# Performance work log

Hardware: AMD Instinct MI355X
Metric: run time of the kernel (lower is better)

## Reference

```python
import jax, jax.numpy as jnp
import numpy as np

N_HEAD = 16
NEG_INF = jnp.float32(-1e30)


def setup_inputs() -> dict:
    key = jax.random.key(0)
    k1, k2, k3 = jax.random.split(key, 3)
    B, T, C = 2, 2048, 1024
    x = jax.random.normal(k1, (B, T, C), dtype=jnp.float32)
    attn_mask = jnp.ones((B, T), dtype=jnp.int32)
    W_qkv = jax.random.normal(k2, (C, 3 * C), dtype=jnp.float32) * (1.0 / np.sqrt(C))
    b_qkv = jnp.zeros((3 * C,), dtype=jnp.float32)
    W_proj = jax.random.normal(k3, (C, C), dtype=jnp.float32) * (1.0 / np.sqrt(C))
    b_proj = jnp.zeros((C,), dtype=jnp.float32)
    return {"x": x, "attn_mask": attn_mask, "W_qkv": W_qkv, "b_qkv": b_qkv,
            "W_proj": W_proj, "b_proj": b_proj}


def reference(x, attn_mask, W_qkv, b_qkv, W_proj, b_proj):
    B, T, C = x.shape
    H = N_HEAD
    hd = C // H
    qkv = x @ W_qkv + b_qkv                       # [B,T,3C]
    q, k, v = jnp.split(qkv, 3, axis=-1)
    q = q.reshape(B, T, H, hd).transpose(0, 2, 1, 3)  # [B,H,T,hd]
    k = k.reshape(B, T, H, hd).transpose(0, 2, 1, 3)
    v = v.reshape(B, T, H, hd).transpose(0, 2, 1, 3)
    att = jnp.einsum('bhqd,bhkd->bhqk', q, k) / jnp.float32(np.sqrt(hd))  # [B,H,T,T]
    causal = jnp.tril(jnp.ones((T, T), dtype=bool))[None, None]           # [1,1,T,T]
    pad = (attn_mask != 0)[:, None, None, :]                              # [B,1,1,T]
    att = jnp.where(causal & pad, att, NEG_INF)
    att = jax.nn.softmax(att, axis=-1)
    y = jnp.einsum('bhqk,bhkd->bhqd', att, v)     # [B,H,T,hd]
    y = y.transpose(0, 2, 1, 3).reshape(B, T, C)
    return y @ W_proj + b_proj
```

## Files before the change

### kernel.cpp

```cpp
#include <hip/hip_runtime.h>

#define T_SEQ 2048
#define NHEAD 16
#define HD 64
#define CDIM 1024

typedef __bf16 bf16x8 __attribute__((ext_vector_type(8)));
typedef float f32x4 __attribute__((ext_vector_type(4)));

union U16x8 { uint4 u4; unsigned short s[8]; bf16x8 b; };

__device__ __forceinline__ float bf2f(unsigned short u) {
    return __uint_as_float(((unsigned int)u) << 16);
}
__device__ __forceinline__ unsigned short f2bf(float f) {
    unsigned int u = __float_as_uint(f);
    u += 0x7fffu + ((u >> 16) & 1u);
    return (unsigned short)(u >> 16);
}
__device__ __forceinline__ unsigned short f2bf_fast(float f) {
    return (unsigned short)((__float_as_uint(f) + 0x8000u) >> 16);
}
__device__ __forceinline__ U16x8 load8f(const float* __restrict__ p) {
    U16x8 r;
    float4 f0 = *(const float4*)p;
    float4 f1 = *(const float4*)(p + 4);
    r.s[0] = f2bf(f0.x); r.s[1] = f2bf(f0.y); r.s[2] = f2bf(f0.z); r.s[3] = f2bf(f0.w);
    r.s[4] = f2bf(f1.x); r.s[5] = f2bf(f1.y); r.s[6] = f2bf(f1.z); r.s[7] = f2bf(f1.w);
    return r;
}

__device__ __forceinline__ void async_copy16(const unsigned short* g, unsigned short* l) {
    __builtin_amdgcn_global_load_lds(
        (const __attribute__((address_space(1))) unsigned int*)g,
        (__attribute__((address_space(3))) unsigned int*)l, 16, 0, 0);
}

#define LOG2E 1.442695040f

#define BAR()    asm volatile("s_barrier" ::: "memory")
#define LGKM0()  asm volatile("s_waitcnt lgkmcnt(0)" ::: "memory")
#define VMC6()   asm volatile("s_waitcnt vmcnt(6)" ::: "memory")
#define VMC0()   asm volatile("s_waitcnt vmcnt(0)" ::: "memory")

__global__ __launch_bounds__(256) void conv_bf16(
    const float* __restrict__ in, unsigned short* __restrict__ out, int n)
{
    const int i = (blockIdx.x * 256 + threadIdx.x) * 8;
    if (i < n) {
        U16x8 o = load8f(&in[i]);
        *(uint4*)&out[i] = o.u4;
    }
}

__global__ __launch_bounds__(256) void transpose_conv(
    const float* __restrict__ in, unsigned short* __restrict__ out, int R, int C)
{
    __shared__ float tile[64][65];
    const int r0 = blockIdx.x * 64;
    const int c0 = blockIdx.y * 64;
    const int tid = threadIdx.x;
    const int rr = tid >> 4;
    const int cc = (tid & 15) * 4;
#pragma unroll
    for (int p = 0; p < 4; ++p) {
        float4 v = *(const float4*)&in[(size_t)(r0 + p * 16 + rr) * C + c0 + cc];
        tile[p * 16 + rr][cc] = v.x;
        tile[p * 16 + rr][cc + 1] = v.y;
        tile[p * 16 + rr][cc + 2] = v.z;
        tile[p * 16 + rr][cc + 3] = v.w;
    }
    __syncthreads();
    const int n = tid >> 2;
    const int s = (tid & 3) * 8;
#pragma unroll
    for (int p = 0; p < 2; ++p) {
        const int k = s + p * 32;
        U16x8 o;
#pragma unroll
        for (int j = 0; j < 8; ++j) o.s[j] = f2bf(tile[k + j][n]);
        *(uint4*)&out[(size_t)(c0 + n) * R + r0 + k] = o.u4;
    }
}

__device__ __forceinline__ void gemm128_core(
    const unsigned short* __restrict__ A,
    const unsigned short* __restrict__ Bt,
    int K, int m0, int n0,
    unsigned short* As, unsigned short* Bs, f32x4 acc[4][4])
{
    const int tid = threadIdx.x;
    const int w = tid >> 6, lane = tid & 63;
    const int ln = lane & 15, quad = lane >> 4;
    const int wm = w >> 1, wn = w & 1;
    const int lr = lane >> 3;
    const int lc = (lane & 7) * 8;

    for (int kb = 0; kb < K; kb += 64) {
        __syncthreads();
#pragma unroll
        for (int i = 0; i < 4; ++i) {
            async_copy16(&A[(size_t)(m0 + w * 32 + i * 8 + lr) * K + kb + lc],
                         &As[(w * 32 + i * 8) * 64]);
            async_copy16(&Bt[(size_t)(n0 + w * 32 + i * 8 + lr) * K + kb + lc],
                         &Bs[(w * 32 + i * 8) * 64]);
        }
        __syncthreads();
#pragma unroll
        for (int kk = 0; kk < 2; ++kk) {
            U16x8 af[4], bff[4];
#pragma unroll
            for (int i = 0; i < 4; ++i)
                af[i].u4 = *(const uint4*)&As[(wm * 64 + i * 16 + ln) * 64 + kk * 32 + quad * 8];
#pragma unroll
            for (int j = 0; j < 4; ++j)
                bff[j].u4 = *(const uint4*)&Bs[(wn * 64 + j * 16 + ln) * 64 + kk * 32 + quad * 8];
#pragma unroll
            for (int i = 0; i < 4; ++i)
#pragma unroll
                for (int j = 0; j < 4; ++j)
                    acc[i][j] = __builtin_amdgcn_mfma_f32_16x16x32_bf16(af[i].b, bff[j].b, acc[i][j], 0, 0, 0);
        }
    }
}


__device__ __forceinline__ void stageA(const unsigned short* __restrict__ A,
                                       unsigned short* buf,
                                       int m0, int t, int unit, int w, int lane)
{
#pragma unroll
    for (int s = 0; s < 2; ++s) {
        const int r0 = s * 128 + unit * 64 + w * 8;
        const int row = r0 + (lane >> 3);
        const int col = (16 * (lane & 7)) ^ ((row & 4) ? 32 : 0);
        const unsigned short* src = A + (size_t)(m0 + row) * CDIM + t * 64 + (col >> 1);
        async_copy16(src, buf + r0 * 64);
    }
}

__device__ __forceinline__ void stageB(const unsigned short* __restrict__ B,
                                       unsigned short* buf,
                                       int n0, int t, int unit, int w, int lane)
{
#pragma unroll
    for (int s = 0; s < 2; ++s) {
        const int slice = s * 8 + w;
        const int r0 = (slice >> 2) * 64 + unit * 32 + (slice & 3) * 8;
        const int row = r0 + (lane >> 3);
        const int col = (16 * (lane & 7)) ^ ((row & 4) ? 32 : 0);
        const unsigned short* src = B + (size_t)(n0 + row) * CDIM + t * 64 + (col >> 1);
        async_copy16(src, buf + r0 * 64);
    }
}

__device__ __forceinline__ void readA(U16x8 af[4][2], const unsigned short* buf,
                                      int wm, int qm, int ln, int quad)
{
#pragma unroll
    for (int i = 0; i < 4; ++i) {
        const int row = wm * 128 + qm * 64 + i * 16 + ln;
        const int sw = (row & 4) ? 32 : 0;
#pragma unroll
        for (int kk = 0; kk < 2; ++kk) {
            const int byt = row * 128 + ((kk * 64 + quad * 16) ^ sw);
            af[i][kk].u4 = *(const uint4*)((const char*)buf + byt);
        }
    }
}

__device__ __forceinline__ void readB(U16x8 bf[2][2], const unsigned short* buf,
                                      int wn, int qn, int ln, int quad)
{
#pragma unroll
    for (int jj = 0; jj < 2; ++jj) {
        const int row = wn * 64 + qn * 32 + jj * 16 + ln;
        const int sw = (row & 4) ? 32 : 0;
#pragma unroll
        for (int kk = 0; kk < 2; ++kk) {
            const int byt = row * 128 + ((kk * 64 + quad * 16) ^ sw);
            bf[jj][kk].u4 = *(const uint4*)((const char*)buf + byt);
        }
    }
}

template<int QM, int QN>
__device__ __forceinline__ void mfma16(f32x4 acc[8][4], const U16x8 af[4][2],
                                       const U16x8 bf[2][2])
{
    __builtin_amdgcn_s_setprio(1);
#pragma unroll
    for (int i = 0; i < 4; ++i)
#pragma unroll
        for (int jj = 0; jj < 2; ++jj)
#pragma unroll
            for (int kk = 0; kk < 2; ++kk)
                acc[QM * 4 + i][QN * 2 + jj] = __builtin_amdgcn_mfma_f32_16x16x32_bf16(
                    af[i][kk].b, bf[jj][kk].b, acc[QM * 4 + i][QN * 2 + jj], 0, 0, 0);
    __builtin_amdgcn_s_setprio(0);
}

__global__ __launch_bounds__(512) void qkv8(
    const unsigned short* __restrict__ Xb,
    const unsigned short* __restrict__ Wt,
    const float* __restrict__ bias,
    unsigned short* __restrict__ Qp,
    unsigned short* __restrict__ Kp,
    unsigned short* __restrict__ Vtp)
{
    __shared__ __align__(1024) unsigned short smem[4][16384];
    unsigned short* Ab0 = smem[0];
    unsigned short* Ab1 = smem[1];
    unsigned short* Bb0 = smem[2];
    unsigned short* Bb1 = smem[3];

    const int tid = threadIdx.x;
    const int w = tid >> 6, lane = tid & 63;
    const int ln = lane & 15, quad = lane >> 4;
    const int wm = w >> 2, wn = w & 3;

    const int bid = blockIdx.x;
    const int swz = (bid & 7) * 24 + (bid >> 3);
    const int nt = swz % 12, mt = swz / 12;
    const int m0 = mt * 256, n0 = nt * 256;

    f32x4 acc[8][4];
#pragma unroll
    for (int i = 0; i < 8; ++i)
#pragma unroll
        for (int j = 0; j < 4; ++j) acc[i][j] = (f32x4){0.f, 0.f, 0.f, 0.f};

    stageA(Xb, Ab0, m0, 0, 0, w, lane);
    stageB(Wt, Bb0, n0, 0, 0, w, lane);
    stageB(Wt, Bb0, n0, 0, 1, w, lane);
    stageA(Xb, Ab0, m0, 0, 1, w, lane);
    stageA(Xb, Ab1, m0, 1, 0, w, lane);
    stageB(Wt, Bb1, n0, 1, 0, w, lane);
    stageB(Wt, Bb1, n0, 1, 1, w, lane);
    VMC6();
    BAR();

    U16x8 af[4][2], bq0[2][2], bq1[2][2];

    for (int j = 0; j < 7; ++j) {
        const int e = 2 * j, o = 2 * j + 1;
        readA(af, Ab0, wm, 0, ln, quad);
        readB(bq0, Bb0, wn, 0, ln, quad);
        stageA(Xb, Ab1, m0, o, 1, w, lane);
        BAR(); LGKM0();
        mfma16<0, 0>(acc, af, bq0);
        LGKM0(); BAR();
        readB(bq1, Bb0, wn, 1, ln, quad);
        stageA(Xb, Ab0, m0, e + 2, 0, w, lane);
        BAR(); LGKM0();
        mfma16<0, 1>(acc, af, bq1);
        LGKM0(); BAR();
        readA(af, Ab0, wm, 1, ln, quad);
        stageB(Wt, Bb0, n0, e + 2, 0, w, lane);
        BAR(); LGKM0();
        mfma16<1, 0>(acc, af, bq0);
        LGKM0(); BAR();
        stageB(Wt, Bb0, n0, e + 2, 1, w, lane);
        BAR();
        mfma16<1, 1>(acc, af, bq1);
        VMC6(); BAR();
        readA(af, Ab1, wm, 0, ln, quad);
        readB(bq0, Bb1, wn, 0, ln, quad);
        stageA(Xb, Ab0, m0, e + 2, 1, w, lane);
        BAR(); LGKM0();
        mfma16<0, 0>(acc, af, bq0);
        LGKM0(); BAR();
        readB(bq1, Bb1, wn, 1, ln, quad);
        stageA(Xb, Ab1, m0, o + 2, 0, w, lane);
        BAR(); LGKM0();
        mfma16<0, 1>(acc, af, bq1);
        LGKM0(); BAR();
        readA(af, Ab1, wm, 1, ln, quad);
        stageB(Wt, Bb1, n0, o + 2, 0, w, lane);
        BAR(); LGKM0();
        mfma16<1, 0>(acc, af, bq0);
        LGKM0(); BAR();
        stageB(Wt, Bb1, n0, o + 2, 1, w, lane);
        BAR();
        mfma16<1, 1>(acc, af, bq1);
        VMC6(); BAR();
    }

    stageA(Xb, Ab1, m0, 15, 1, w, lane);
    VMC0(); BAR();

    readA(af, Ab0, wm, 0, ln, quad);
    readB(bq0, Bb0, wn, 0, ln, quad);
    readB(bq1, Bb0, wn, 1, ln, quad);
    mfma16<0, 0>(acc, af, bq0);
    mfma16<0, 1>(acc, af, bq1);
    readA(af, Ab0, wm, 1, ln, quad);
    mfma16<1, 0>(acc, af, bq0);
    mfma16<1, 1>(acc, af, bq1);

    readA(af, Ab1, wm, 0, ln, quad);
    readB(bq0, Bb1, wn, 0, ln, quad);
    readB(bq1, Bb1, wn, 1, ln, quad);
    mfma16<0, 0>(acc, af, bq0);
    mfma16<0, 1>(acc, af, bq1);
    readA(af, Ab1, wm, 1, ln, quad);
    mfma16<1, 0>(acc, af, bq0);
    mfma16<1, 1>(acc, af, bq1);

    const int which = n0 >> 10;
    float bv[4];
#pragma unroll
    for (int jj = 0; jj < 4; ++jj) bv[jj] = bias[n0 + wn * 64 + jj * 16 + ln];

    if (which < 2) {
        unsigned short* dst = (which == 0) ? Qp : Kp;
#pragma unroll
        for (int jj = 0; jj < 4; ++jj) {
            const int n = n0 + wn * 64 + jj * 16 + ln;
            const int h = (n >> 6) & 15, d = n & 63;
#pragma unroll
            for (int i = 0; i < 8; ++i)
#pragma unroll
                for (int r = 0; r < 4; ++r) {
                    const int m = m0 + wm * 128 + i * 16 + quad * 4 + r;
                    const int b = m >> 11, tt = m & 2047;
                    dst[(((size_t)(b * NHEAD + h) * T_SEQ) + tt) * HD + d] =
                        f2bf(acc[i][jj][r] + bv[jj]);
                }
        }
    } else {
#pragma unroll
        for (int jj = 0; jj < 4; ++jj) {
            const int n = n0 + wn * 64 + jj * 16 + ln;
            const int c = n - 2048;
#pragma unroll
            for (int i = 0; i < 8; ++i) {
                const int m00 = m0 + wm * 128 + i * 16 + quad * 4;
                const int b = m00 >> 11, tt = m00 & 2047;
                ushort4 pk;
                pk.x = f2bf(acc[i][jj][0] + bv[jj]);
                pk.y = f2bf(acc[i][jj][1] + bv[jj]);
                pk.z = f2bf(acc[i][jj][2] + bv[jj]);
                pk.w = f2bf(acc[i][jj][3] + bv[jj]);
                *(ushort4*)&Vtp[(size_t)(b * 1024 + c) * T_SEQ + tt] = pk;
            }
        }
    }
}

__global__ __launch_bounds__(256) void proj_gemm(
    const unsigned short* __restrict__ Yin,
    const unsigned short* __restrict__ Wt,
    const float* __restrict__ bias,
    float* __restrict__ out)
{
    __shared__ unsigned short As[128 * 64];
    __shared__ unsigned short Bs[128 * 64];
    const int m0 = blockIdx.y * 128;
    const int n0 = blockIdx.x * 128;

    f32x4 acc[4][4];
#pragma unroll
    for (int i = 0; i < 4; ++i)
#pragma unroll
        for (int j = 0; j < 4; ++j) acc[i][j] = (f32x4){0.f, 0.f, 0.f, 0.f};

    gemm128_core(Yin, Wt, CDIM, m0, n0, As, Bs, acc);

    const int tid = threadIdx.x;
    const int w = tid >> 6, lane = tid & 63;
    const int ln = lane & 15, quad = lane >> 4;
    const int wm = w >> 1, wn = w & 1;

#pragma unroll
    for (int j = 0; j < 4; ++j) {
        const int n = n0 + wn * 64 + j * 16 + ln;
        const float bv = bias[n];
#pragma unroll
        for (int i = 0; i < 4; ++i)
#pragma unroll
            for (int r = 0; r < 4; ++r) {
                const int m = m0 + wm * 64 + i * 16 + quad * 4 + r;
                out[(size_t)m * CDIM + n] = acc[i][j][r] + bv;
            }
    }
}

#define ATT_STRIDE 72

__global__ __launch_bounds__(256) void flash_attn(
    const unsigned short* __restrict__ Qp,
    const unsigned short* __restrict__ Kp,
    const unsigned short* __restrict__ Vtp,
    const int* __restrict__ mask,
    unsigned short* __restrict__ Y)
{
    __shared__ unsigned short Ks[64 * ATT_STRIDE];
    __shared__ unsigned short Vs[64 * ATT_STRIDE];
    __shared__ unsigned short Ps[64 * ATT_STRIDE];
    __shared__ float mask_f[64];

    const int bh = blockIdx.x;
    const int qt = (T_SEQ / 64 - 1) - blockIdx.y;
    const int b = bh >> 4, h = bh & 15;
    const int tid = threadIdx.x;
    const int w = tid >> 6, lane = tid & 63;
    const int ln = lane & 15, quad = lane >> 4;
    const int row8 = tid >> 3, seg = tid & 7;
    const size_t base = (size_t)bh * T_SEQ * HD;
    const int q0 = qt * 64;

    U16x8 qf[2];
    {
        const unsigned short* qrow = &Qp[base + (size_t)(q0 + w * 16 + ln) * HD];
        qf[0].u4 = *(const uint4*)&qrow[quad * 8];
        qf[1].u4 = *(const uint4*)&qrow[32 + quad * 8];
    }

    f32x4 o[4];
#pragma unroll
    for (int n = 0; n < 4; ++n) o[n] = (f32x4){0.f, 0.f, 0.f, 0.f};
    float m_i[4] = {-3.0e38f, -3.0e38f, -3.0e38f, -3.0e38f};
    float l_i[4] = {0.f, 0.f, 0.f, 0.f};

    uint4 kr0, kr1, vr0, vr1;
    float mf = 0.f;
    {
        const unsigned short* kp0 = &Kp[base + (size_t)row8 * HD + seg * 8];
        kr0 = *(const uint4*)kp0;
        kr1 = *(const uint4*)(kp0 + 32 * HD);
        const unsigned short* vp0 = &Vtp[base + (size_t)row8 * T_SEQ + seg * 8];
        vr0 = *(const uint4*)vp0;
        vr1 = *(const uint4*)(vp0 + 32 * T_SEQ);
        if (tid < 64) mf = mask[b * T_SEQ + tid] ? 0.f : -1.0e30f;
    }

    for (int j = 0; j <= qt; ++j) {
        __syncthreads();
        *(uint4*)&Ks[row8 * ATT_STRIDE + seg * 8] = kr0;
        *(uint4*)&Ks[(row8 + 32) * ATT_STRIDE + seg * 8] = kr1;
        *(uint4*)&Vs[row8 * ATT_STRIDE + seg * 8] = vr0;
        *(uint4*)&Vs[(row8 + 32) * ATT_STRIDE + seg * 8] = vr1;
        if (tid < 64) mask_f[tid] = mf;
        __syncthreads();

        if (j < qt) {
            const unsigned short* kp0 = &Kp[base + (size_t)((j + 1) * 64 + row8) * HD + seg * 8];
            kr0 = *(const uint4*)kp0;
            kr1 = *(const uint4*)(kp0 + 32 * HD);
            const unsigned short* vp0 = &Vtp[base + (size_t)row8 * T_SEQ + (j + 1) * 64 + seg * 8];
            vr0 = *(const uint4*)vp0;
            vr1 = *(const uint4*)(vp0 + 32 * T_SEQ);
            if (tid < 64) mf = mask[b * T_SEQ + (j + 1) * 64 + tid] ? 0.f : -1.0e30f;
        }

        const bool diag = (j == qt);

        f32x4 sc[4];
#pragma unroll
        for (int t = 0; t < 4; ++t) sc[t] = (f32x4){0.f, 0.f, 0.f, 0.f};
#pragma unroll
        for (int t = 0; t < 4; ++t) {
            if (diag && t > w) continue;
#pragma unroll
            for (int s = 0; s < 2; ++s) {
                U16x8 kb;
                kb.u4 = *(const uint4*)&Ks[(t * 16 + ln) * ATT_STRIDE + s * 32 + quad * 8];
                sc[t] = __builtin_amdgcn_mfma_f32_16x16x32_bf16(qf[s].b, kb.b, sc[t], 0, 0, 0);
            }
        }

        float rm[4] = {-3.0e38f, -3.0e38f, -3.0e38f, -3.0e38f};
#pragma unroll
        for (int t = 0; t < 4; ++t) {
            if (diag && t > w) {
#pragma unroll
                for (int i = 0; i < 4; ++i) sc[t][i] = -1.0e30f;
            } else {
                const float madd = mask_f[t * 16 + ln];
                const bool edge = diag && (t == w);
#pragma unroll
                for (int i = 0; i < 4; ++i) {
                    float v = fmaf(sc[t][i], 0.125f, madd);
                    if (edge && ln > quad * 4 + i) v = -1.0e30f;
                    sc[t][i] = v;
                    rm[i] = fmaxf(rm[i], v);
                }
            }
        }
#pragma unroll
        for (int i = 0; i < 4; ++i) {
            rm[i] = fmaxf(rm[i], __shfl_xor(rm[i], 1));
            rm[i] = fmaxf(rm[i], __shfl_xor(rm[i], 2));
            rm[i] = fmaxf(rm[i], __shfl_xor(rm[i], 4));
            rm[i] = fmaxf(rm[i], __shfl_xor(rm[i], 8));
        }

        float alpha[4], mlog[4];
#pragma unroll
        for (int i = 0; i < 4; ++i) {
            const float nm = fmaxf(m_i[i], rm[i]);
            alpha[i] = __builtin_amdgcn_exp2f((m_i[i] - nm) * LOG2E);
            m_i[i] = nm;
            mlog[i] = nm * LOG2E;
        }
        float rsp[4] = {0.f, 0.f, 0.f, 0.f};
#pragma unroll
        for (int t = 0; t < 4; ++t)
#pragma unroll
            for (int i = 0; i < 4; ++i) {
                const float p = __builtin_amdgcn_exp2f(fmaf(sc[t][i], LOG2E, -mlog[i]));
                sc[t][i] = p;
                rsp[i] += p;
            }
#pragma unroll
        for (int i = 0; i < 4; ++i) l_i[i] = l_i[i] * alpha[i] + rsp[i];
#pragma unroll
        for (int n = 0; n < 4; ++n)
#pragma unroll
            for (int i = 0; i < 4; ++i) o[n][i] *= alpha[i];

#pragma unroll
        for (int t = 0; t < 4; ++t)
#pragma unroll
            for (int i = 0; i < 4; ++i)
                Ps[(w * 16 + quad * 4 + i) * ATT_STRIDE + t * 16 + ln] = f2bf_fast(sc[t][i]);

        U16x8 pa[2];
        pa[0].u4 = *(const uint4*)&Ps[(w * 16 + ln) * ATT_STRIDE + quad * 8];
        pa[1].u4 = *(const uint4*)&Ps[(w * 16 + ln) * ATT_STRIDE + 32 + quad * 8];

#pragma unroll
        for (int n = 0; n < 4; ++n)
#pragma unroll
            for (int s = 0; s < 2; ++s) {
                U16x8 vb;
                vb.u4 = *(const uint4*)&Vs[(n * 16 + ln) * ATT_STRIDE + s * 32 + quad * 8];
                o[n] = __builtin_amdgcn_mfma_f32_16x16x32_bf16(pa[s].b, vb.b, o[n], 0, 0, 0);
            }
    }

#pragma unroll
    for (int i = 0; i < 4; ++i) {
        float l = l_i[i];
        l += __shfl_xor(l, 1);
        l += __shfl_xor(l, 2);
        l += __shfl_xor(l, 4);
        l += __shfl_xor(l, 8);
        const float inv = 1.0f / l;
        const size_t row = (size_t)(b * T_SEQ + q0 + w * 16 + quad * 4 + i);
#pragma unroll
        for (int n = 0; n < 4; ++n)
            Y[row * CDIM + h * HD + n * 16 + ln] = f2bf(o[n][i] * inv);
    }
}

extern "C" void kernel_launch(void* const* d_in, const int* in_sizes, int n_in,
                              void* d_out, int out_size, void* d_ws, size_t ws_size,
                              hipStream_t stream)
{
    const float* X     = (const float*)d_in[0];
    const int*   mask  = (const int*)d_in[1];
    const float* Wqkv  = (const float*)d_in[2];
    const float* bqkv  = (const float*)d_in[3];
    const float* Wproj = (const float*)d_in[4];
    const float* bproj = (const float*)d_in[5];
    float* out = (float*)d_out;

    const size_t per = (size_t)2 * NHEAD * T_SEQ * HD;
    unsigned short* Qp     = (unsigned short*)d_ws;
    unsigned short* Kp     = Qp + per;
    unsigned short* Vtp    = Kp + per;
    unsigned short* Xb     = Vtp + per;
    unsigned short* Yp     = Xb;
    unsigned short* Wqkvt  = Xb + per;
    unsigned short* Wprojt = Wqkvt + (size_t)3 * CDIM * CDIM;

    conv_bf16<<<2048, 256, 0, stream>>>(X, Xb, 4 * 1024 * 1024);
    transpose_conv<<<dim3(16, 48), 256, 0, stream>>>(Wqkv, Wqkvt, CDIM, 3 * CDIM);
    transpose_conv<<<dim3(16, 16), 256, 0, stream>>>(Wproj, Wprojt, CDIM, CDIM);

    qkv8<<<192, 512, 0, stream>>>(Xb, Wqkvt, bqkv, Qp, Kp, Vtp);
    flash_attn<<<dim3(2 * NHEAD, T_SEQ / 64), 256, 0, stream>>>(Qp, Kp, Vtp, mask, Yp);
    proj_gemm<<<dim3(8, 32), 256, 0, stream>>>(Yp, Wprojt, bproj, out);
}
```

Before: 216.9 us.

## Rewrite flash attention with 32x32 MFMA, 128-row query tiles and register P

Replaces the flash attention kernel with one that processes 128 query rows per block (32 per wave) using 32x32x16 bf16 MFMA. It computes S^T so the probabilities can be packed to bf16 and moved into the A-operand layout with v_permlane32_swap, removing the LDS round trip for P. It also adds XOR-swizzled LDS for K/V, skips mask arithmetic when a ballot shows the tile is unmasked, and uses a lazy rescale that only updates the running max when it grows by more than 8. The grid shrinks to 512 blocks with fewer but longer blocks, which risks load imbalance and higher register pressure.

```diff
diff --git a/kernel.cpp b/kernel.cpp
--- a/kernel.cpp
+++ b/kernel.cpp
@@ -7,6 +7,7 @@
 
 typedef __bf16 bf16x8 __attribute__((ext_vector_type(8)));
 typedef float f32x4 __attribute__((ext_vector_type(4)));
+typedef float f32x16 __attribute__((ext_vector_type(16)));
 
 union U16x8 { uint4 u4; unsigned short s[8]; bf16x8 b; };
 
@@ -17,9 +18,6 @@
     unsigned int u = __float_as_uint(f);
     u += 0x7fffu + ((u >> 16) & 1u);
     return (unsigned short)(u >> 16);
-}
-__device__ __forceinline__ unsigned short f2bf_fast(float f) {
-    return (unsigned short)((__float_as_uint(f) + 0x8000u) >> 16);
 }
 __device__ __forceinline__ U16x8 load8f(const float* __restrict__ p) {
     U16x8 r;
@@ -43,6 +41,15 @@
 #define VMC6()   asm volatile("s_waitcnt vmcnt(6)" ::: "memory")
 #define VMC0()   asm volatile("s_waitcnt vmcnt(0)" ::: "memory")
 
+__device__ __forceinline__ unsigned int cvtpk_bf16(float lo, float hi) {
+    unsigned int r;
+    asm("v_cvt_pk_bf16_f32 %0, %1, %2" : "=v"(r) : "v"(lo), "v"(hi));
+    return r;
+}
+__device__ __forceinline__ void plane32swap(unsigned int &x, unsigned int &y) {
+    asm("v_permlane32_swap_b32 %0, %1" : "+v"(x), "+v"(y));
+}
+
 __global__ __launch_bounds__(256) void conv_bf16(
     const float* __restrict__ in, unsigned short* __restrict__ out, int n)
 {
@@ -123,7 +130,6 @@
         }
     }
 }
-
 
 __device__ __forceinline__ void stageA(const unsigned short* __restrict__ A,
                                        unsigned short* buf,
@@ -386,42 +392,49 @@
     }
 }
 
-#define ATT_STRIDE 72
-
-__global__ __launch_bounds__(256) void flash_attn(
+
+__device__ __forceinline__ int swz(int row, int slot) {
+    return row * 64 + ((slot ^ (row & 7)) << 3);
+}
+
+__global__ __launch_bounds__(256) void flash_attn32(
     const unsigned short* __restrict__ Qp,
     const unsigned short* __restrict__ Kp,
     const unsigned short* __restrict__ Vtp,
     const int* __restrict__ mask,
     unsigned short* __restrict__ Y)
 {
-    __shared__ unsigned short Ks[64 * ATT_STRIDE];
-    __shared__ unsigned short Vs[64 * ATT_STRIDE];
-    __shared__ unsigned short Ps[64 * ATT_STRIDE];
-    __shared__ float mask_f[64];
+    __shared__ unsigned short Ks[64 * 64];
+    __shared__ unsigned short Vs[64 * 64];
+    __shared__ float mask_arr[64];
+    __shared__ float als[4][32];
+    __shared__ int flagu;
 
     const int bh = blockIdx.x;
-    const int qt = (T_SEQ / 64 - 1) - blockIdx.y;
+    const int qb = 15 - blockIdx.y;
     const int b = bh >> 4, h = bh & 15;
     const int tid = threadIdx.x;
     const int w = tid >> 6, lane = tid & 63;
-    const int ln = lane & 15, quad = lane >> 4;
+    const int l31 = lane & 31, hi = lane >> 5;
     const int row8 = tid >> 3, seg = tid & 7;
     const size_t base = (size_t)bh * T_SEQ * HD;
-    const int q0 = qt * 64;
-
-    U16x8 qf[2];
+    const int qB = qb * 128;
+    const int qw0 = qB + w * 32;
+    const int qv = qw0 + l31;
+    const int jlast = 2 * qb + 1;
+
+    U16x8 qf[4];
     {
-        const unsigned short* qrow = &Qp[base + (size_t)(q0 + w * 16 + ln) * HD];
-        qf[0].u4 = *(const uint4*)&qrow[quad * 8];
-        qf[1].u4 = *(const uint4*)&qrow[32 + quad * 8];
-    }
-
-    f32x4 o[4];
-#pragma unroll
-    for (int n = 0; n < 4; ++n) o[n] = (f32x4){0.f, 0.f, 0.f, 0.f};
-    float m_i[4] = {-3.0e38f, -3.0e38f, -3.0e38f, -3.0e38f};
-    float l_i[4] = {0.f, 0.f, 0.f, 0.f};
+        const unsigned short* qrow = &Qp[base + (size_t)qv * HD];
+#pragma unroll
+        for (int c = 0; c < 4; ++c)
+            qf[c].u4 = *(const uint4*)&qrow[c * 16 + hi * 8];
+    }
+
+    f32x16 oA0, oA1;
+#pragma unroll
+    for (int r = 0; r < 16; ++r) { oA0[r] = 0.f; oA1[r] = 0.f; }
+    float m_r = -3.0e38f, mL = 0.f, l_r = 0.f;
 
     uint4 kr0, kr1, vr0, vr1;
     float mf = 0.f;
@@ -435,16 +448,22 @@
         if (tid < 64) mf = mask[b * T_SEQ + tid] ? 0.f : -1.0e30f;
     }
 
-    for (int j = 0; j <= qt; ++j) {
+    for (int j = 0; j <= jlast; ++j) {
         __syncthreads();
-        *(uint4*)&Ks[row8 * ATT_STRIDE + seg * 8] = kr0;
-        *(uint4*)&Ks[(row8 + 32) * ATT_STRIDE + seg * 8] = kr1;
-        *(uint4*)&Vs[row8 * ATT_STRIDE + seg * 8] = vr0;
-        *(uint4*)&Vs[(row8 + 32) * ATT_STRIDE + seg * 8] = vr1;
-        if (tid < 64) mask_f[tid] = mf;
+        *(uint4*)&Ks[swz(row8, seg)]      = kr0;
+        *(uint4*)&Ks[swz(row8 + 32, seg)] = kr1;
+        *(uint4*)&Vs[swz(row8, seg)]      = vr0;
+        *(uint4*)&Vs[swz(row8 + 32, seg)] = vr1;
+        if (w == 0) {
+            const int k = lane;
+            const int idx = ((k >> 2) & 1) * 32 + (k >> 5) * 16 + ((k & 31) >> 3) * 4 + (k & 3);
+            mask_arr[idx] = mf;
+            const unsigned long long bb = __ballot(mf == 0.f);
+            if (lane == 0) flagu = (bb == 0xFFFFFFFFFFFFFFFFull) ? 0 : 1;
+        }
         __syncthreads();
 
-        if (j < qt) {
+        if (j < jlast) {
             const unsigned short* kp0 = &Kp[base + (size_t)((j + 1) * 64 + row8) * HD + seg * 8];
             kr0 = *(const uint4*)kp0;
             kr1 = *(const uint4*)(kp0 + 32 * HD);
@@ -454,104 +473,129 @@
             if (tid < 64) mf = mask[b * T_SEQ + (j + 1) * 64 + tid] ? 0.f : -1.0e30f;
         }
 
-        const bool diag = (j == qt);
-
-        f32x4 sc[4];
-#pragma unroll
-        for (int t = 0; t < 4; ++t) sc[t] = (f32x4){0.f, 0.f, 0.f, 0.f};
-#pragma unroll
-        for (int t = 0; t < 4; ++t) {
-            if (diag && t > w) continue;
-#pragma unroll
-            for (int s = 0; s < 2; ++s) {
-                U16x8 kb;
-                kb.u4 = *(const uint4*)&Ks[(t * 16 + ln) * ATT_STRIDE + s * 32 + quad * 8];
-                sc[t] = __builtin_amdgcn_mfma_f32_16x16x32_bf16(qf[s].b, kb.b, sc[t], 0, 0, 0);
-            }
-        }
-
-        float rm[4] = {-3.0e38f, -3.0e38f, -3.0e38f, -3.0e38f};
-#pragma unroll
-        for (int t = 0; t < 4; ++t) {
-            if (diag && t > w) {
-#pragma unroll
-                for (int i = 0; i < 4; ++i) sc[t][i] = -1.0e30f;
+        const bool skipw = (j * 64 > qw0 + 31);
+        if (!skipw) {
+            const bool edge = (j * 64 + 63 > qw0);
+            const int anymask = flagu;
+
+            f32x16 sc0, sc1;
+#pragma unroll
+            for (int r = 0; r < 16; ++r) { sc0[r] = 0.f; sc1[r] = 0.f; }
+#pragma unroll
+            for (int c = 0; c < 4; ++c) {
+                U16x8 ka0, ka1;
+                const int r0 = l31, r1 = 32 + l31;
+                ka0.u4 = *(const uint4*)&Ks[r0 * 64 + (((2 * c + hi) ^ (r0 & 7)) << 3)];
+                ka1.u4 = *(const uint4*)&Ks[r1 * 64 + (((2 * c + hi) ^ (r1 & 7)) << 3)];
+                sc0 = __builtin_amdgcn_mfma_f32_32x32x16_bf16(ka0.b, qf[c].b, sc0, 0, 0, 0);
+                sc1 = __builtin_amdgcn_mfma_f32_32x32x16_bf16(ka1.b, qf[c].b, sc1, 0, 0, 0);
+            }
+
+            if (anymask) {
+#pragma unroll
+                for (int g = 0; g < 4; ++g) {
+                    const f32x4 m0v = *(const f32x4*)&mask_arr[hi * 32 + g * 4];
+                    const f32x4 m1v = *(const f32x4*)&mask_arr[hi * 32 + 16 + g * 4];
+#pragma unroll
+                    for (int t = 0; t < 4; ++t) {
+                        sc0[g * 4 + t] = fmaf(sc0[g * 4 + t], 0.125f, m0v[t]);
+                        sc1[g * 4 + t] = fmaf(sc1[g * 4 + t], 0.125f, m1v[t]);
+                    }
+                }
             } else {
-                const float madd = mask_f[t * 16 + ln];
-                const bool edge = diag && (t == w);
-#pragma unroll
-                for (int i = 0; i < 4; ++i) {
-                    float v = fmaf(sc[t][i], 0.125f, madd);
-                    if (edge && ln > quad * 4 + i) v = -1.0e30f;
-                    sc[t][i] = v;
-                    rm[i] = fmaxf(rm[i], v);
+#pragma unroll
+                for (int r = 0; r < 16; ++r) {
+                    sc0[r] *= 0.125f;
+                    sc1[r] *= 0.125f;
                 }
             }
-        }
-#pragma unroll
-        for (int i = 0; i < 4; ++i) {
-            rm[i] = fmaxf(rm[i], __shfl_xor(rm[i], 1));
-            rm[i] = fmaxf(rm[i], __shfl_xor(rm[i], 2));
-            rm[i] = fmaxf(rm[i], __shfl_xor(rm[i], 4));
-            rm[i] = fmaxf(rm[i], __shfl_xor(rm[i], 8));
-        }
-
-        float alpha[4], mlog[4];
-#pragma unroll
-        for (int i = 0; i < 4; ++i) {
-            const float nm = fmaxf(m_i[i], rm[i]);
-            alpha[i] = __builtin_amdgcn_exp2f((m_i[i] - nm) * LOG2E);
-            m_i[i] = nm;
-            mlog[i] = nm * LOG2E;
-        }
-        float rsp[4] = {0.f, 0.f, 0.f, 0.f};
-#pragma unroll
-        for (int t = 0; t < 4; ++t)
-#pragma unroll
-            for (int i = 0; i < 4; ++i) {
-                const float p = __builtin_amdgcn_exp2f(fmaf(sc[t][i], LOG2E, -mlog[i]));
-                sc[t][i] = p;
-                rsp[i] += p;
-            }
-#pragma unroll
-        for (int i = 0; i < 4; ++i) l_i[i] = l_i[i] * alpha[i] + rsp[i];
-#pragma unroll
-        for (int n = 0; n < 4; ++n)
-#pragma unroll
-            for (int i = 0; i < 4; ++i) o[n][i] *= alpha[i];
-
-#pragma unroll
-        for (int t = 0; t < 4; ++t)
-#pragma unroll
-            for (int i = 0; i < 4; ++i)
-                Ps[(w * 16 + quad * 4 + i) * ATT_STRIDE + t * 16 + ln] = f2bf_fast(sc[t][i]);
-
-        U16x8 pa[2];
-        pa[0].u4 = *(const uint4*)&Ps[(w * 16 + ln) * ATT_STRIDE + quad * 8];
-        pa[1].u4 = *(const uint4*)&Ps[(w * 16 + ln) * ATT_STRIDE + 32 + quad * 8];
-
-#pragma unroll
-        for (int n = 0; n < 4; ++n)
-#pragma unroll
-            for (int s = 0; s < 2; ++s) {
-                U16x8 vb;
-                vb.u4 = *(const uint4*)&Vs[(n * 16 + ln) * ATT_STRIDE + s * 32 + quad * 8];
-                o[n] = __builtin_amdgcn_mfma_f32_16x16x32_bf16(pa[s].b, vb.b, o[n], 0, 0, 0);
-            }
-    }
-
-#pragma unroll
-    for (int i = 0; i < 4; ++i) {
-        float l = l_i[i];
-        l += __shfl_xor(l, 1);
-        l += __shfl_xor(l, 2);
-        l += __shfl_xor(l, 4);
-        l += __shfl_xor(l, 8);
-        const float inv = 1.0f / l;
-        const size_t row = (size_t)(b * T_SEQ + q0 + w * 16 + quad * 4 + i);
-#pragma unroll
-        for (int n = 0; n < 4; ++n)
-            Y[row * CDIM + h * HD + n * 16 + ln] = f2bf(o[n][i] * inv);
+            if (edge) {
+#pragma unroll
+                for (int r = 0; r < 16; ++r) {
+                    const int krow = (r & 3) + 8 * (r >> 2) + 4 * hi;
+                    if (j * 64 + krow > qv)      sc0[r] = -1.0e30f;
+                    if (j * 64 + 32 + krow > qv) sc1[r] = -1.0e30f;
+                }
+            }
+
+            float tm = -3.0e38f;
+#pragma unroll
+            for (int r = 0; r < 16; ++r)
+                tm = fmaxf(tm, fmaxf(sc0[r], sc1[r]));
+            tm = fmaxf(tm, __shfl_xor(tm, 32));
+
+            if (__any(tm > m_r + 8.f)) {
+                const float mn = fmaxf(m_r, tm);
+                const float a = __builtin_amdgcn_exp2f((m_r - mn) * LOG2E);
+                m_r = mn; mL = mn * LOG2E;
+                l_r *= a;
+                if (hi == 0) als[w][l31] = a;
+                f32x4 av[4];
+#pragma unroll
+                for (int g = 0; g < 4; ++g)
+                    av[g] = *(const f32x4*)&als[w][g * 8 + hi * 4];
+#pragma unroll
+                for (int r = 0; r < 16; ++r) {
+                    const float aa = av[r >> 2][r & 3];
+                    oA0[r] *= aa; oA1[r] *= aa;
+                }
+            }
+
+            float ps = 0.f;
+#pragma unroll
+            for (int r = 0; r < 16; ++r) {
+                const float p0 = __builtin_amdgcn_exp2f(fmaf(sc0[r], LOG2E, -mL));
+                const float p1 = __builtin_amdgcn_exp2f(fmaf(sc1[r], LOG2E, -mL));
+                sc0[r] = p0; sc1[r] = p1;
+                ps += p0 + p1;
+            }
+            l_r += ps;
+
+#pragma unroll
+            for (int c = 0; c < 4; ++c) {
+                const int rb = (c & 1) * 8;
+                unsigned int x0, y0, x1, y1;
+                if (c < 2) {
+                    x0 = cvtpk_bf16(sc0[rb + 0], sc0[rb + 1]);
+                    y0 = cvtpk_bf16(sc0[rb + 4], sc0[rb + 5]);
+                    x1 = cvtpk_bf16(sc0[rb + 2], sc0[rb + 3]);
+                    y1 = cvtpk_bf16(sc0[rb + 6], sc0[rb + 7]);
+                } else {
+                    x0 = cvtpk_bf16(sc1[rb + 0], sc1[rb + 1]);
+                    y0 = cvtpk_bf16(sc1[rb + 4], sc1[rb + 5]);
+                    x1 = cvtpk_bf16(sc1[rb + 2], sc1[rb + 3]);
+                    y1 = cvtpk_bf16(sc1[rb + 6], sc1[rb + 7]);
+                }
+                plane32swap(x0, y0);
+                plane32swap(x1, y1);
+                U16x8 pa;
+                pa.u4 = make_uint4(x0, x1, y0, y1);
+                {
+                    const int vr_0 = l31, vr_1 = 32 + l31;
+                    U16x8 vb0, vb1;
+                    vb0.u4 = *(const uint4*)&Vs[vr_0 * 64 + (((2 * c + hi) ^ (vr_0 & 7)) << 3)];
+                    vb1.u4 = *(const uint4*)&Vs[vr_1 * 64 + (((2 * c + hi) ^ (vr_1 & 7)) << 3)];
+                    oA0 = __builtin_amdgcn_mfma_f32_32x32x16_bf16(pa.b, vb0.b, oA0, 0, 0, 0);
+                    oA1 = __builtin_amdgcn_mfma_f32_32x32x16_bf16(pa.b, vb1.b, oA1, 0, 0, 0);
+                }
+            }
+        }
+    }
+
+    const float lt = l_r + __shfl_xor(l_r, 32);
+    if (hi == 0) als[w][l31] = 1.0f / lt;
+    f32x4 lv[4];
+#pragma unroll
+    for (int g = 0; g < 4; ++g)
+        lv[g] = *(const f32x4*)&als[w][g * 8 + hi * 4];
+
+#pragma unroll
+    for (int r = 0; r < 16; ++r) {
+        const int q = qw0 + (r & 3) + 8 * (r >> 2) + 4 * hi;
+        const float sl = lv[r >> 2][r & 3];
+        const size_t row = (size_t)(b * T_SEQ + q);
+        Y[row * CDIM + h * HD + l31]      = f2bf(oA0[r] * sl);
+        Y[row * CDIM + h * HD + 32 + l31] = f2bf(oA1[r] * sl);
     }
 }
 
@@ -580,7 +624,7 @@
     transpose_conv<<<dim3(16, 48), 256, 0, stream>>>(Wqkv, Wqkvt, CDIM, 3 * CDIM);
     transpose_conv<<<dim3(16, 16), 256, 0, stream>>>(Wproj, Wprojt, CDIM, CDIM);
 
-    qkv8<<<192, 512, 0, stream>>>(Xb, Wqkvt, bqkv, Qp, Kp, Vtp);
-    flash_attn<<<dim3(2 * NHEAD, T_SEQ / 64), 256, 0, stream>>>(Qp, Kp, Vtp, mask, Yp);
+    qkv8<<<768 / 4, 512, 0, stream>>>(Xb, Wqkvt, bqkv, Qp, Kp, Vtp);
+    flash_attn32<<<dim3(2 * NHEAD, 16), 256, 0, stream>>>(Qp, Kp, Vtp, mask, Yp);
     proj_gemm<<<dim3(8, 32), 256, 0, stream>>>(Yp, Wprojt, bproj, out);
 }
```

Result: no change. 218.0 us (+0.5%).

## Rewrite flash attention as per-warp 32-row tiles with register-only K/V and P

Applied to the files above, without the earlier changes.

Replaces the block-cooperative flash attention, which staged K/V and P through LDS with block barriers, with a per-wavefront design. Each wave owns 32 query rows of a different head, loads K and transposed V straight from global memory into registers with double buffering, and uses 32x32x16 MFMA with S computed transposed. P is converted in registers via cvt_pk_bf16 and permlane32_swap, so the LDS round trip and barriers are gone. It also adds lazy rescaling (only when the max grows by more than 8), a fast path when the mask is all valid, and s_setprio around the MFMAs. The cost is heavier register use and uncoached global loads with no K/V reuse across waves in a block.

```diff
diff --git a/kernel.cpp b/kernel.cpp
--- a/kernel.cpp
+++ b/kernel.cpp
@@ -7,6 +7,7 @@
 
 typedef __bf16 bf16x8 __attribute__((ext_vector_type(8)));
 typedef float f32x4 __attribute__((ext_vector_type(4)));
+typedef float f32x16 __attribute__((ext_vector_type(16)));
 
 union U16x8 { uint4 u4; unsigned short s[8]; bf16x8 b; };
 
@@ -17,9 +18,6 @@
     unsigned int u = __float_as_uint(f);
     u += 0x7fffu + ((u >> 16) & 1u);
     return (unsigned short)(u >> 16);
-}
-__device__ __forceinline__ unsigned short f2bf_fast(float f) {
-    return (unsigned short)((__float_as_uint(f) + 0x8000u) >> 16);
 }
 __device__ __forceinline__ U16x8 load8f(const float* __restrict__ p) {
     U16x8 r;
@@ -43,6 +41,15 @@
 #define VMC6()   asm volatile("s_waitcnt vmcnt(6)" ::: "memory")
 #define VMC0()   asm volatile("s_waitcnt vmcnt(0)" ::: "memory")
 
+__device__ __forceinline__ unsigned int cvtpk_bf16(float lo, float hi) {
+    unsigned int r;
+    asm("v_cvt_pk_bf16_f32 %0, %1, %2" : "=v"(r) : "v"(lo), "v"(hi));
+    return r;
+}
+__device__ __forceinline__ void plane32swap(unsigned int &x, unsigned int &y) {
+    asm("v_permlane32_swap_b32 %0, %1" : "+v"(x), "+v"(y));
+}
+
 __global__ __launch_bounds__(256) void conv_bf16(
     const float* __restrict__ in, unsigned short* __restrict__ out, int n)
 {
@@ -123,7 +130,6 @@
         }
     }
 }
-
 
 __device__ __forceinline__ void stageA(const unsigned short* __restrict__ A,
                                        unsigned short* buf,
@@ -386,172 +392,146 @@
     }
 }
 
-#define ATT_STRIDE 72
-
-__global__ __launch_bounds__(256) void flash_attn(
+
+#define FW_LOADSET(S, t)                                                              \
+    {                                                                                 \
+        const int _r = (t) * 32 + l31;                                                \
+        k##S[0].u4 = *(const uint4*)&Kb[(size_t)_r * HD + hi * 8];                    \
+        k##S[1].u4 = *(const uint4*)&Kb[(size_t)_r * HD + 16 + hi * 8];               \
+        k##S[2].u4 = *(const uint4*)&Kb[(size_t)_r * HD + 32 + hi * 8];               \
+        k##S[3].u4 = *(const uint4*)&Kb[(size_t)_r * HD + 48 + hi * 8];               \
+        v##S[0].u4 = *(const uint4*)&Vb[(size_t)l31 * T_SEQ + (t) * 32 + hi * 8];     \
+        v##S[1].u4 = *(const uint4*)&Vb[(size_t)l31 * T_SEQ + (t) * 32 + 16 + hi * 8];\
+        v##S[2].u4 = *(const uint4*)&Vb[(size_t)(l31 + 32) * T_SEQ + (t) * 32 + hi * 8];\
+        v##S[3].u4 = *(const uint4*)&Vb[(size_t)(l31 + 32) * T_SEQ + (t) * 32 + 16 + hi * 8];\
+        m##S = mrow[(t) * 32 + l31];                                                  \
+    }
+
+#define FW_BODY(S, kb)                                                                \
+    {                                                                                 \
+        const bool allv = (__ballot(m##S != 0) == 0xFFFFFFFFFFFFFFFFull);             \
+        f32x16 sc;                                                                    \
+        _Pragma("unroll")                                                             \
+        for (int r = 0; r < 16; ++r) sc[r] = 0.f;                                     \
+        __builtin_amdgcn_s_setprio(1);                                                \
+        sc = __builtin_amdgcn_mfma_f32_32x32x16_bf16(k##S[0].b, qf[0].b, sc, 0, 0, 0);\
+        sc = __builtin_amdgcn_mfma_f32_32x32x16_bf16(k##S[1].b, qf[1].b, sc, 0, 0, 0);\
+        sc = __builtin_amdgcn_mfma_f32_32x32x16_bf16(k##S[2].b, qf[2].b, sc, 0, 0, 0);\
+        sc = __builtin_amdgcn_mfma_f32_32x32x16_bf16(k##S[3].b, qf[3].b, sc, 0, 0, 0);\
+        __builtin_amdgcn_s_setprio(0);                                                \
+        if (allv) {                                                                   \
+            _Pragma("unroll")                                                         \
+            for (int r = 0; r < 16; ++r) sc[r] *= 0.125f;                             \
+        } else {                                                                      \
+            const float mv0 = m##S ? 0.f : -1.0e30f;                                  \
+            _Pragma("unroll")                                                         \
+            for (int r = 0; r < 16; ++r)                                              \
+                sc[r] = fmaf(sc[r], 0.125f,                                           \
+                             __shfl(mv0, (r & 3) + 8 * (r >> 2) + 4 * hi));           \
+        }                                                                             \
+        if ((kb) == c) {                                                              \
+            _Pragma("unroll")                                                         \
+            for (int r = 0; r < 16; ++r)                                              \
+                if ((r & 3) + 8 * (r >> 2) + 4 * hi > l31) sc[r] = -1.0e30f;          \
+        }                                                                             \
+        float tm = -3.0e38f;                                                          \
+        _Pragma("unroll")                                                             \
+        for (int r = 0; r < 16; ++r) tm = fmaxf(tm, sc[r]);                           \
+        tm = fmaxf(tm, __shfl_xor(tm, 32));                                           \
+        if (__any(tm > m_r + 8.f)) {                                                  \
+            const float mn = fmaxf(m_r, tm);                                          \
+            const float a = __builtin_amdgcn_exp2f((m_r - mn) * LOG2E);               \
+            m_r = mn; mL = mn * LOG2E;                                                \
+            l_r *= a;                                                                 \
+            _Pragma("unroll")                                                         \
+            for (int r = 0; r < 16; ++r) {                                            \
+                const float ar = __shfl(a, (r & 3) + 8 * (r >> 2) + 4 * hi);          \
+                oA0[r] *= ar; oA1[r] *= ar;                                           \
+            }                                                                         \
+        }                                                                             \
+        float ps = 0.f;                                                               \
+        _Pragma("unroll")                                                             \
+        for (int r = 0; r < 16; ++r) {                                                \
+            const float p = __builtin_amdgcn_exp2f(fmaf(sc[r], LOG2E, -mL));          \
+            sc[r] = p; ps += p;                                                       \
+        }                                                                             \
+        l_r += ps;                                                                    \
+        unsigned int x0, y0, x1, y1;                                                  \
+        U16x8 pa0, pa1;                                                               \
+        x0 = cvtpk_bf16(sc[0], sc[1]); x1 = cvtpk_bf16(sc[2], sc[3]);                 \
+        y0 = cvtpk_bf16(sc[4], sc[5]); y1 = cvtpk_bf16(sc[6], sc[7]);                 \
+        plane32swap(x0, y0); plane32swap(x1, y1);                                     \
+        pa0.u4 = make_uint4(x0, x1, y0, y1);                                          \
+        x0 = cvtpk_bf16(sc[8], sc[9]);  x1 = cvtpk_bf16(sc[10], sc[11]);              \
+        y0 = cvtpk_bf16(sc[12], sc[13]); y1 = cvtpk_bf16(sc[14], sc[15]);             \
+        plane32swap(x0, y0); plane32swap(x1, y1);                                     \
+        pa1.u4 = make_uint4(x0, x1, y0, y1);                                          \
+        __builtin_amdgcn_s_setprio(1);                                                \
+        oA0 = __builtin_amdgcn_mfma_f32_32x32x16_bf16(pa0.b, v##S[0].b, oA0, 0, 0, 0);\
+        oA0 = __builtin_amdgcn_mfma_f32_32x32x16_bf16(pa1.b, v##S[1].b, oA0, 0, 0, 0);\
+        oA1 = __builtin_amdgcn_mfma_f32_32x32x16_bf16(pa0.b, v##S[2].b, oA1, 0, 0, 0);\
+        oA1 = __builtin_amdgcn_mfma_f32_32x32x16_bf16(pa1.b, v##S[3].b, oA1, 0, 0, 0);\
+        __builtin_amdgcn_s_setprio(0);                                                \
+    }
+
+__global__ __launch_bounds__(256, 2) void flash_warp(
     const unsigned short* __restrict__ Qp,
     const unsigned short* __restrict__ Kp,
     const unsigned short* __restrict__ Vtp,
     const int* __restrict__ mask,
     unsigned short* __restrict__ Y)
 {
-    __shared__ unsigned short Ks[64 * ATT_STRIDE];
-    __shared__ unsigned short Vs[64 * ATT_STRIDE];
-    __shared__ unsigned short Ps[64 * ATT_STRIDE];
-    __shared__ float mask_f[64];
-
-    const int bh = blockIdx.x;
-    const int qt = (T_SEQ / 64 - 1) - blockIdx.y;
-    const int b = bh >> 4, h = bh & 15;
+    const int bid = blockIdx.x;
     const int tid = threadIdx.x;
     const int w = tid >> 6, lane = tid & 63;
-    const int ln = lane & 15, quad = lane >> 4;
-    const int row8 = tid >> 3, seg = tid & 7;
+    const int l31 = lane & 31, hi = lane >> 5;
+
+    const int bh = (bid & 7) + 8 * w;
+    const int b = bh >> 4, h = bh & 15;
+    const int c = 63 - (bid >> 3);
+    const int q0 = c * 32;
     const size_t base = (size_t)bh * T_SEQ * HD;
-    const int q0 = qt * 64;
-
-    U16x8 qf[2];
+
+    const unsigned short* Kb = Kp + base;
+    const unsigned short* Vb = Vtp + base;
+    const int* mrow = mask + b * T_SEQ;
+
+    U16x8 qf[4];
     {
-        const unsigned short* qrow = &Qp[base + (size_t)(q0 + w * 16 + ln) * HD];
-        qf[0].u4 = *(const uint4*)&qrow[quad * 8];
-        qf[1].u4 = *(const uint4*)&qrow[32 + quad * 8];
-    }
-
-    f32x4 o[4];
-#pragma unroll
-    for (int n = 0; n < 4; ++n) o[n] = (f32x4){0.f, 0.f, 0.f, 0.f};
-    float m_i[4] = {-3.0e38f, -3.0e38f, -3.0e38f, -3.0e38f};
-    float l_i[4] = {0.f, 0.f, 0.f, 0.f};
-
-    uint4 kr0, kr1, vr0, vr1;
-    float mf = 0.f;
-    {
-        const unsigned short* kp0 = &Kp[base + (size_t)row8 * HD + seg * 8];
-        kr0 = *(const uint4*)kp0;
-        kr1 = *(const uint4*)(kp0 + 32 * HD);
-        const unsigned short* vp0 = &Vtp[base + (size_t)row8 * T_SEQ + seg * 8];
-        vr0 = *(const uint4*)vp0;
-        vr1 = *(const uint4*)(vp0 + 32 * T_SEQ);
-        if (tid < 64) mf = mask[b * T_SEQ + tid] ? 0.f : -1.0e30f;
-    }
-
-    for (int j = 0; j <= qt; ++j) {
-        __syncthreads();
-        *(uint4*)&Ks[row8 * ATT_STRIDE + seg * 8] = kr0;
-        *(uint4*)&Ks[(row8 + 32) * ATT_STRIDE + seg * 8] = kr1;
-        *(uint4*)&Vs[row8 * ATT_STRIDE + seg * 8] = vr0;
-        *(uint4*)&Vs[(row8 + 32) * ATT_STRIDE + seg * 8] = vr1;
-        if (tid < 64) mask_f[tid] = mf;
-        __syncthreads();
-
-        if (j < qt) {
-            const unsigned short* kp0 = &Kp[base + (size_t)((j + 1) * 64 + row8) * HD + seg * 8];
-            kr0 = *(const uint4*)kp0;
-            kr1 = *(const uint4*)(kp0 + 32 * HD);
-            const unsigned short* vp0 = &Vtp[base + (size_t)row8 * T_SEQ + (j + 1) * 64 + seg * 8];
-            vr0 = *(const uint4*)vp0;
-            vr1 = *(const uint4*)(vp0 + 32 * T_SEQ);
-            if (tid < 64) mf = mask[b * T_SEQ + (j + 1) * 64 + tid] ? 0.f : -1.0e30f;
-        }
-
-        const bool diag = (j == qt);
-
-        f32x4 sc[4];
-#pragma unroll
-        for (int t = 0; t < 4; ++t) sc[t] = (f32x4){0.f, 0.f, 0.f, 0.f};
-#pragma unroll
-        for (int t = 0; t < 4; ++t) {
-            if (diag && t > w) continue;
-#pragma unroll
-            for (int s = 0; s < 2; ++s) {
-                U16x8 kb;
-                kb.u4 = *(const uint4*)&Ks[(t * 16 + ln) * ATT_STRIDE + s * 32 + quad * 8];
-                sc[t] = __builtin_amdgcn_mfma_f32_16x16x32_bf16(qf[s].b, kb.b, sc[t], 0, 0, 0);
-            }
-        }
-
-        float rm[4] = {-3.0e38f, -3.0e38f, -3.0e38f, -3.0e38f};
-#pragma unroll
-        for (int t = 0; t < 4; ++t) {
-            if (diag && t > w) {
-#pragma unroll
-                for (int i = 0; i < 4; ++i) sc[t][i] = -1.0e30f;
-            } else {
-                const float madd = mask_f[t * 16 + ln];
-                const bool edge = diag && (t == w);
-#pragma unroll
-                for (int i = 0; i < 4; ++i) {
-                    float v = fmaf(sc[t][i], 0.125f, madd);
-                    if (edge && ln > quad * 4 + i) v = -1.0e30f;
-                    sc[t][i] = v;
-                    rm[i] = fmaxf(rm[i], v);
-                }
-            }
-        }
-#pragma unroll
-        for (int i = 0; i < 4; ++i) {
-            rm[i] = fmaxf(rm[i], __shfl_xor(rm[i], 1));
-            rm[i] = fmaxf(rm[i], __shfl_xor(rm[i], 2));
-            rm[i] = fmaxf(rm[i], __shfl_xor(rm[i], 4));
-            rm[i] = fmaxf(rm[i], __shfl_xor(rm[i], 8));
-        }
-
-        float alpha[4], mlog[4];
-#pragma unroll
-        for (int i = 0; i < 4; ++i) {
-            const float nm = fmaxf(m_i[i], rm[i]);
-            alpha[i] = __builtin_amdgcn_exp2f((m_i[i] - nm) * LOG2E);
-            m_i[i] = nm;
-            mlog[i] = nm * LOG2E;
-        }
-        float rsp[4] = {0.f, 0.f, 0.f, 0.f};
-#pragma unroll
-        for (int t = 0; t < 4; ++t)
-#pragma unroll
-            for (int i = 0; i < 4; ++i) {
-                const float p = __builtin_amdgcn_exp2f(fmaf(sc[t][i], LOG2E, -mlog[i]));
-                sc[t][i] = p;
-                rsp[i] += p;
-            }
-#pragma unroll
-        for (int i = 0; i < 4; ++i) l_i[i] = l_i[i] * alpha[i] + rsp[i];
-#pragma unroll
-        for (int n = 0; n < 4; ++n)
-#pragma unroll
-            for (int i = 0; i < 4; ++i) o[n][i] *= alpha[i];
-
-#pragma unroll
-        for (int t = 0; t < 4; ++t)
-#pragma unroll
-            for (int i = 0; i < 4; ++i)
-                Ps[(w * 16 + quad * 4 + i) * ATT_STRIDE + t * 16 + ln] = f2bf_fast(sc[t][i]);
-
-        U16x8 pa[2];
-        pa[0].u4 = *(const uint4*)&Ps[(w * 16 + ln) * ATT_STRIDE + quad * 8];
-        pa[1].u4 = *(const uint4*)&Ps[(w * 16 + ln) * ATT_STRIDE + 32 + quad * 8];
-
-#pragma unroll
-        for (int n = 0; n < 4; ++n)
-#pragma unroll
-            for (int s = 0; s < 2; ++s) {
-                U16x8 vb;
-                vb.u4 = *(const uint4*)&Vs[(n * 16 + ln) * ATT_STRIDE + s * 32 + quad * 8];
-                o[n] = __builtin_amdgcn_mfma_f32_16x16x32_bf16(pa[s].b, vb.b, o[n], 0, 0, 0);
-            }
-    }
-
-#pragma unroll
-    for (int i = 0; i < 4; ++i) {
-        float l = l_i[i];
-        l += __shfl_xor(l, 1);
-        l += __shfl_xor(l, 2);
-        l += __shfl_xor(l, 4);
-        l += __shfl_xor(l, 8);
-        const float inv = 1.0f / l;
-        const size_t row = (size_t)(b * T_SEQ + q0 + w * 16 + quad * 4 + i);
-#pragma unroll
-        for (int n = 0; n < 4; ++n)
-            Y[row * CDIM + h * HD + n * 16 + ln] = f2bf(o[n][i] * inv);
+        const unsigned short* qrow = &Qp[base + (size_t)(q0 + l31) * HD];
+#pragma unroll
+        for (int c4 = 0; c4 < 4; ++c4)
+            qf[c4].u4 = *(const uint4*)&qrow[c4 * 16 + hi * 8];
+    }
+
+    f32x16 oA0, oA1;
+#pragma unroll
+    for (int r = 0; r < 16; ++r) { oA0[r] = 0.f; oA1[r] = 0.f; }
+    float m_r = -3.0e38f, mL = 0.f, l_r = 0.f;
+
+    U16x8 kA[4], vA[4], kB[4], vB[4];
+    int mA, mB;
+
+    FW_LOADSET(A, 0);
+    int kb = 0;
+    while (true) {
+        if (kb < c) FW_LOADSET(B, kb + 1);
+        FW_BODY(A, kb);
+        ++kb; if (kb > c) break;
+        if (kb < c) FW_LOADSET(A, kb + 1);
+        FW_BODY(B, kb);
+        ++kb; if (kb > c) break;
+    }
+
+    const float lt = l_r + __shfl_xor(l_r, 32);
+    const float inv = 1.0f / lt;
+#pragma unroll
+    for (int r = 0; r < 16; ++r) {
+        const int crow = (r & 3) + 8 * (r >> 2) + 4 * hi;
+        const float ir = __shfl(inv, crow);
+        const size_t row = (size_t)(b * T_SEQ + q0 + crow);
+        Y[row * CDIM + h * HD + l31]      = f2bf(oA0[r] * ir);
+        Y[row * CDIM + h * HD + 32 + l31] = f2bf(oA1[r] * ir);
     }
 }
 
@@ -581,6 +561,6 @@
     transpose_conv<<<dim3(16, 16), 256, 0, stream>>>(Wproj, Wprojt, CDIM, CDIM);
 
     qkv8<<<192, 512, 0, stream>>>(Xb, Wqkvt, bqkv, Qp, Kp, Vtp);
-    flash_attn<<<dim3(2 * NHEAD, T_SEQ / 64), 256, 0, stream>>>(Qp, Kp, Vtp, mask, Yp);
+    flash_warp<<<512, 256, 0, stream>>>(Qp, Kp, Vtp, mask, Yp);
     proj_gemm<<<dim3(8, 32), 256, 0, stream>>>(Yp, Wprojt, bproj, out);
 }
```

After: 251.5 us. 1.16x slower.
